# Kernel optimization log

Hardware: AMD Instinct MI355X
Metric: run time of the kernel (lower is better)

## Reference

```python
import jax, jax.numpy as jnp
import numpy as np

MARGIN = 0.3
BIG = 1e6  # matches the 1000000.0 additive mask in the torch code


def setup_inputs() -> dict:
    key = jax.random.key(0)
    k1, k2 = jax.random.split(key)
    embeddings = jax.random.normal(k1, (4096, 512), dtype=jnp.float32)
    labels = jax.random.randint(k2, (4096,), 0, 512)
    return {"embeddings": embeddings, "labels": labels}


def reference(embeddings, labels):
    # Pairwise euclidean distances (torch.cdist p=2) via the GEMM identity,
    # clamped before sqrt for numerical safety on the zero diagonal.
    sq = jnp.sum(embeddings * embeddings, axis=1)                      # [N]
    d2 = sq[:, None] + sq[None, :] - 2.0 * (embeddings @ embeddings.T)  # [N, N]
    dist = jnp.sqrt(jnp.maximum(d2, 1e-12))

    pos_mask = labels[None, :] == labels[:, None]   # [N, N] bool
    neg_mask = ~pos_mask

    # Hardest positive per anchor (self-distance 0 is harmless under max).
    hp = jnp.max(dist * pos_mask.astype(dist.dtype), axis=1)           # [N]

    # Semi-hard negatives: hp < d(a, n) < hp + margin, different label.
    semi_hard = (dist > hp[:, None]) & (dist < hp[:, None] + MARGIN) & neg_mask
    has_semi_hard = jnp.sum(semi_hard) > 0

    # Fallback: hardest (farthest) negative; semi-hard branch: closest semi-hard.
    hn_fallback = jnp.max(dist * neg_mask.astype(dist.dtype), axis=1)
    hn_semi = jnp.min(dist + (1.0 - semi_hard.astype(dist.dtype)) * BIG, axis=1)
    hn = jnp.where(has_semi_hard, hn_semi, hn_fallback)                # [N]

    triplet = jax.nn.relu(hp - hn + MARGIN)                            # [N]
    num_valid = jnp.sum((triplet > 0).astype(triplet.dtype))
    loss = jnp.where(num_valid > 0,
                     jnp.sum(triplet) / jnp.maximum(num_valid, 1.0),
                     jnp.mean(triplet))
    return loss
```

## Files before the change

kernel.cpp:

```cpp
#include <hip/hip_runtime.h>
#include <math.h>


constexpr float MARGIN = 0.3f;

typedef _Float16 half8    __attribute__((ext_vector_type(8)));
typedef float    floatx16 __attribute__((ext_vector_type(16)));

#define GLD_LDS16(gp, lp)                                                              \
    __builtin_amdgcn_global_load_lds(                                                  \
        (const __attribute__((address_space(1))) void*)(gp),                           \
        (__attribute__((address_space(3))) void*)(lp), 16, 0, 0)

__global__ __launch_bounds__(256)
void prep_kernel(const float* __restrict__ e, _Float16* __restrict__ pan,
                 float* __restrict__ sq, unsigned int* __restrict__ hp,
                 unsigned int* __restrict__ hn_fall, unsigned int* __restrict__ hn_semi,
                 unsigned int* __restrict__ bars, int N, int D) {
    __shared__ float red[256];
    if (blockIdx.x == 0 && threadIdx.x < 32) bars[threadIdx.x * 32] = 0u;
    const int r0  = blockIdx.x * 8;
    const int p   = r0 >> 7;
    const int rl  = r0 & 127;
    const int r   = threadIdx.x & 7;
    const int c8  = threadIdx.x >> 3;
    const int row = r0 + r;
    const float* er = e + (size_t)row * D;
    float s = 0.f;
    #pragma unroll
    for (int it = 0; it < 2; ++it) {
        const int kw = c8 + it * 32;
        const float4 x0 = *(const float4*)&er[kw * 8];
        const float4 x1 = *(const float4*)&er[kw * 8 + 4];
        const float xv[8] = {x0.x, x0.y, x0.z, x0.w, x1.x, x1.y, x1.z, x1.w};
        half8 hi, lo;
        #pragma unroll
        for (int jj = 0; jj < 8; ++jj) {
            _Float16 h = (_Float16)xv[jj];
            hi[jj] = h;
            lo[jj] = (_Float16)(xv[jj] - (float)h);
            s += xv[jj] * xv[jj];
        }
        *(half8*)&pan[((size_t)(p * 128 + kw) * 128 + rl + r) * 8]      = hi;
        *(half8*)&pan[((size_t)(p * 128 + 64 + kw) * 128 + rl + r) * 8] = lo;
    }
    red[threadIdx.x] = s;
    __syncthreads();
    if (threadIdx.x < 8) {
        float t = 0.f;
        #pragma unroll
        for (int c = 0; c < 32; ++c) t += red[threadIdx.x + 8 * c];
        const int rw = r0 + threadIdx.x;
        sq[rw]      = t;
        hp[rw]      = 0u;
        hn_fall[rw] = 0u;
        hn_semi[rw] = 0x7f800000u;
    }
}

__global__ __launch_bounds__(512, 2)
void fused_kernel(const _Float16* __restrict__ pan, const int* __restrict__ labels,
                  const float* __restrict__ sq,
                  unsigned int* __restrict__ hp,
                  unsigned int* __restrict__ hn_fall,
                  unsigned int* __restrict__ hn_semi,
                  unsigned int* __restrict__ bars,
                  float* __restrict__ out,
                  int N, int D, unsigned int nrowblocks, unsigned int nblocks) {
    __shared__ __attribute__((aligned(16))) _Float16 S[2][32768];
    __shared__ float sq_r[256], sq_c[256], hp_r[256];
    __shared__ int   lab_r[256], lab_c[256];
    __shared__ int   lastflag;

    const int tid  = threadIdx.x;
    const int lane = tid & 63;
    const int wave = tid >> 6;
    const int wr   = (wave >> 2) * 128;
    const int wcol = (wave & 3) * 64;
    const int mrow = lane & 31;
    const int half_id = lane >> 5;

    const int j  = blockIdx.x & 7;
    const int i  = blockIdx.x >> 3;
    const int px = (j & 3) * 4 + (i & 3);
    const int py = (j >> 2) * 8 + (i >> 2);
    const int rowBase = py * 256;
    const int colBase = px * 256;

    if (tid < 256) {
        sq_r[tid]  = sq[rowBase + tid];
        lab_r[tid] = labels[rowBase + tid];
    } else {
        const int t2 = tid - 256;
        sq_c[t2]  = sq[colBase + t2];
        lab_c[t2] = labels[colBase + t2];
    }

    floatx16 acc[2][4];
    #pragma unroll
    for (int b = 0; b < 2; ++b)
        #pragma unroll
        for (int a = 0; a < 4; ++a)
            #pragma unroll
            for (int r = 0; r < 16; ++r) acc[b][a][r] = 0.f;

    auto stage_slab = [&](int nxt, int t, int u) {
        const int s = wave * 8 + u;
        int kcl, pp, rowin, lofs;
        if (s < 32) {
            kcl = s >> 2; const int rq = s & 3;
            pp    = 2 * py + (rq >> 1);
            rowin = (rq & 1) * 64 + lane;
            lofs  = (kcl * 256 + rq * 64) * 8;
        } else {
            const int u2 = s - 32;
            kcl = u2 >> 2; const int cq = u2 & 3;
            pp    = 2 * px + (cq >> 1);
            rowin = (cq & 1) * 64 + lane;
            lofs  = 16384 + (kcl * 256 + cq * 64) * 8;
        }
        const int kc = (kcl < 4) ? (4 * t + kcl) : (64 + 4 * t + (kcl - 4));
        const _Float16* g = pan + ((size_t)(pp * 128 + kc) * 128 + rowin) * 8;
        GLD_LDS16(g, &S[nxt][lofs]);
    };

    #pragma unroll
    for (int u = 0; u < 8; ++u) stage_slab(0, 0, u);
    __syncthreads();

    #pragma unroll 1
    for (int t = 0; t < 16; ++t) {
        const int cur = t & 1, nxt = cur ^ 1;
        const _Float16* Sc = &S[cur][0];
        half8 ah[4], bh[2];
        #pragma unroll
        for (int ph = 0; ph < 4; ++ph) {
            const int kbase = (ph >> 1) * 2 + (ph & 1) * 4;
            half8 av[4], bv[2];
            #pragma unroll
            for (int ai = 0; ai < 4; ++ai)
                av[ai] = *(const half8*)&Sc[((kbase + half_id) * 256 + wr + ai * 32 + mrow) * 8];
            #pragma unroll
            for (int bj = 0; bj < 2; ++bj)
                bv[bj] = *(const half8*)&Sc[16384 + ((kbase + half_id) * 256 + wcol + bj * 32 + mrow) * 8];
            if (t + 1 < 16) {
                stage_slab(nxt, t + 1, 2 * ph);
                stage_slab(nxt, t + 1, 2 * ph + 1);
            }
            asm volatile("" ::: "memory");
            __builtin_amdgcn_s_barrier();
            asm volatile("" ::: "memory");
            __builtin_amdgcn_s_setprio(1);
            if ((ph & 1) == 0) {
                #pragma unroll
                for (int bj = 0; bj < 2; ++bj)
                    #pragma unroll
                    for (int ai = 0; ai < 4; ++ai)
                        acc[bj][ai] = __builtin_amdgcn_mfma_f32_32x32x16_f16(
                            bv[bj], av[ai], acc[bj][ai], 0, 0, 0);
                #pragma unroll
                for (int ai = 0; ai < 4; ++ai) ah[ai] = av[ai];
                bh[0] = bv[0]; bh[1] = bv[1];
            } else {
                #pragma unroll
                for (int bj = 0; bj < 2; ++bj)
                    #pragma unroll
                    for (int ai = 0; ai < 4; ++ai)
                        acc[bj][ai] = __builtin_amdgcn_mfma_f32_32x32x16_f16(
                            bh[bj], av[ai], acc[bj][ai], 0, 0, 0);
                #pragma unroll
                for (int bj = 0; bj < 2; ++bj)
                    #pragma unroll
                    for (int ai = 0; ai < 4; ++ai)
                        acc[bj][ai] = __builtin_amdgcn_mfma_f32_32x32x16_f16(
                            bv[bj], ah[ai], acc[bj][ai], 0, 0, 0);
            }
            __builtin_amdgcn_s_setprio(0);
            if (ph == 3) { asm volatile("s_waitcnt vmcnt(0)" ::: "memory"); }
            asm volatile("" ::: "memory");
            __builtin_amdgcn_s_barrier();
            asm volatile("" ::: "memory");
        }
    }

    float sqr[4]; int labr[4];
    #pragma unroll
    for (int ai = 0; ai < 4; ++ai) {
        sqr[ai]  = sq_r[wr + ai * 32 + mrow];
        labr[ai] = lab_r[wr + ai * 32 + mrow];
    }

    #pragma unroll
    for (int ai = 0; ai < 4; ++ai) {
        float vp = 0.f, vn = 0.f;
        #pragma unroll
        for (int bj = 0; bj < 2; ++bj) {
            #pragma unroll
            for (int r = 0; r < 16; ++r) {
                const int c = wcol + bj * 32 + (r & 3) + 8 * (r >> 2) + 4 * half_id;
                float d = sqrtf(fmaxf(sqr[ai] + sq_c[c] - 2.0f * acc[bj][ai][r], 1e-12f));
                const bool pos = (labr[ai] == lab_c[c]);
                vp = fmaxf(vp, pos ? d : 0.f);
                vn = fmaxf(vn, pos ? 0.f : d);
            }
        }
        vp = fmaxf(vp, __shfl_xor(vp, 32, 64));
        vn = fmaxf(vn, __shfl_xor(vn, 32, 64));
        if (half_id == 0) {
            atomicMax(&hp[rowBase + wr + ai * 32 + mrow],      __float_as_uint(vp));
            atomicMax(&hn_fall[rowBase + wr + ai * 32 + mrow], __float_as_uint(vn));
        }
    }

    __syncthreads();
    unsigned int* ctr = &bars[py * 32];
    if (tid == 0) {
        __threadfence();
        atomicAdd(ctr, 1u);
        while (__hip_atomic_load(ctr, __ATOMIC_ACQUIRE, __HIP_MEMORY_SCOPE_AGENT)
               < nrowblocks)
            __builtin_amdgcn_s_sleep(32);
    }
    __syncthreads();
    if (tid < 256)
        hp_r[tid] = __uint_as_float(__hip_atomic_load(&hp[rowBase + tid],
                                    __ATOMIC_RELAXED, __HIP_MEMORY_SCOPE_AGENT));
    __syncthreads();

    #pragma unroll
    for (int ai = 0; ai < 4; ++ai) {
        const float hpv = hp_r[wr + ai * 32 + mrow];
        float vm = __builtin_inff();
        #pragma unroll
        for (int bj = 0; bj < 2; ++bj) {
            #pragma unroll
            for (int r = 0; r < 16; ++r) {
                const int c = wcol + bj * 32 + (r & 3) + 8 * (r >> 2) + 4 * half_id;
                float d = sqrtf(fmaxf(sqr[ai] + sq_c[c] - 2.0f * acc[bj][ai][r], 1e-12f));
                const bool cand = (labr[ai] != lab_c[c]) && (d > hpv);
                vm = fminf(vm, cand ? d : __builtin_inff());
            }
        }
        vm = fminf(vm, __shfl_xor(vm, 32, 64));
        if (half_id == 0)
            atomicMin(&hn_semi[rowBase + wr + ai * 32 + mrow], __float_as_uint(vm));
    }

    __syncthreads();
    if (tid == 0) {
        __threadfence();
        unsigned int old = atomicAdd(&bars[992], 1u);
        lastflag = (old == nblocks - 1) ? 1 : 0;
    }
    __syncthreads();
    if (!lastflag) return;
    if (tid == 0) __threadfence();
    __syncthreads();

    float* FS = (float*)&S[0][0];
    int*   IC = (int*)(FS + 512);
    int*   IA = IC + 512;
    int any = 0;
    for (int r = tid; r < N; r += 512) {
        float h  = __uint_as_float(__hip_atomic_load(&hp[r],      __ATOMIC_RELAXED, __HIP_MEMORY_SCOPE_AGENT));
        float hs = __uint_as_float(__hip_atomic_load(&hn_semi[r], __ATOMIC_RELAXED, __HIP_MEMORY_SCOPE_AGENT));
        any |= (hs < h + MARGIN) ? 1 : 0;
    }
    IA[tid] = any;
    __syncthreads();
    for (int s = 256; s; s >>= 1) {
        if (tid < s) IA[tid] |= IA[tid + s];
        __syncthreads();
    }
    const bool has_semi = IA[0] != 0;
    float sum = 0.f; int valid = 0;
    for (int r = tid; r < N; r += 512) {
        float h  = __uint_as_float(__hip_atomic_load(&hp[r], __ATOMIC_RELAXED, __HIP_MEMORY_SCOPE_AGENT));
        float hn = has_semi
            ? __uint_as_float(__hip_atomic_load(&hn_semi[r], __ATOMIC_RELAXED, __HIP_MEMORY_SCOPE_AGENT))
            : __uint_as_float(__hip_atomic_load(&hn_fall[r], __ATOMIC_RELAXED, __HIP_MEMORY_SCOPE_AGENT));
        float t = fmaxf(h - hn + MARGIN, 0.f);
        if (!(t > 0.f)) t = 0.f;
        sum += t;
        valid += (t > 0.f) ? 1 : 0;
    }
    FS[tid] = sum; IC[tid] = valid;
    __syncthreads();
    for (int s = 256; s; s >>= 1) {
        if (tid < s) { FS[tid] += FS[tid + s]; IC[tid] += IC[tid + s]; }
        __syncthreads();
    }
    if (tid == 0) {
        float total = FS[0]; int v = IC[0];
        out[0] = (v > 0) ? (total / (float)v) : (total / (float)N);
    }
}

extern "C" void kernel_launch(void* const* d_in, const int* in_sizes, int n_in,
                              void* d_out, int out_size, void* d_ws, size_t ws_size,
                              hipStream_t stream) {
    const float* e      = (const float*)d_in[0];
    const int*   labels = (const int*)d_in[1];
    const int N = in_sizes[1];
    const int D = in_sizes[0] / N;
    float* out = (float*)d_out;

    float*        sq      = (float*)d_ws;
    unsigned int* hp      = (unsigned int*)d_ws + N;
    unsigned int* hn_fall = hp + N;
    unsigned int* hn_semi = hn_fall + N;
    unsigned int* bars    = hn_semi + N;

    const size_t small_bytes = ((size_t)(4 * N + 1024) * 4 + 255) & ~(size_t)255;
    _Float16* pan = (_Float16*)((char*)d_ws + small_bytes);

    prep_kernel<<<N / 8, 256, 0, stream>>>(e, pan, sq, hp, hn_fall, hn_semi, bars, N, D);

    const int ntx = N / 256, nty = N / 256;
    fused_kernel<<<ntx * nty, 512, 0, stream>>>(pan, labels, sq, hp, hn_fall, hn_semi,
                                                bars, out, N, D,
                                                (unsigned)ntx, (unsigned)(ntx * nty));
}
```

Measured before the change: 140.1 us.

## Use 4-wave blocks with 128x128 per-wave tiles and whole-slab prefetch

Halves the block size to 256 threads so each wave computes a 128x128 output sub-tile (4x4 MFMA accumulators) instead of 128x64. The next K-slab is now issued all at once at the top of each iteration, and the fine-grained per-phase barriers are replaced by a single wait and barrier per iteration. The goal is more MFMA reuse per LDS read and less synchronisation. The cost is twice the accumulator registers per wave and lower occupancy (launch bounds 256,1), which may reduce latency hiding.

```diff
diff --git a/kernel.cpp b/kernel.cpp
--- a/kernel.cpp
+++ b/kernel.cpp
@@ -58,7 +58,7 @@
     }
 }
 
-__global__ __launch_bounds__(512, 2)
+__global__ __launch_bounds__(256, 1)
 void fused_kernel(const _Float16* __restrict__ pan, const int* __restrict__ labels,
                   const float* __restrict__ sq,
                   unsigned int* __restrict__ hp,
@@ -75,8 +75,8 @@
     const int tid  = threadIdx.x;
     const int lane = tid & 63;
     const int wave = tid >> 6;
-    const int wr   = (wave >> 2) * 128;
-    const int wcol = (wave & 3) * 64;
+    const int wr   = (wave >> 1) * 128;
+    const int wcol = (wave & 1) * 128;
     const int mrow = lane & 31;
     const int half_id = lane >> 5;
 
@@ -87,25 +87,21 @@
     const int rowBase = py * 256;
     const int colBase = px * 256;
 
-    if (tid < 256) {
-        sq_r[tid]  = sq[rowBase + tid];
-        lab_r[tid] = labels[rowBase + tid];
-    } else {
-        const int t2 = tid - 256;
-        sq_c[t2]  = sq[colBase + t2];
-        lab_c[t2] = labels[colBase + t2];
-    }
-
-    floatx16 acc[2][4];
-    #pragma unroll
-    for (int b = 0; b < 2; ++b)
+    sq_r[tid]  = sq[rowBase + tid];
+    lab_r[tid] = labels[rowBase + tid];
+    sq_c[tid]  = sq[colBase + tid];
+    lab_c[tid] = labels[colBase + tid];
+
+    floatx16 acc[4][4];
+    #pragma unroll
+    for (int b = 0; b < 4; ++b)
         #pragma unroll
         for (int a = 0; a < 4; ++a)
             #pragma unroll
             for (int r = 0; r < 16; ++r) acc[b][a][r] = 0.f;
 
-    auto stage_slab = [&](int nxt, int t, int u) {
-        const int s = wave * 8 + u;
+    auto stage_slab = [&](int buf, int t, int u) {
+        const int s = wave * 16 + u;
         int kcl, pp, rowin, lofs;
         if (s < 32) {
             kcl = s >> 2; const int rq = s & 3;
@@ -121,66 +117,59 @@
         }
         const int kc = (kcl < 4) ? (4 * t + kcl) : (64 + 4 * t + (kcl - 4));
         const _Float16* g = pan + ((size_t)(pp * 128 + kc) * 128 + rowin) * 8;
-        GLD_LDS16(g, &S[nxt][lofs]);
+        GLD_LDS16(g, &S[buf][lofs]);
     };
 
     #pragma unroll
-    for (int u = 0; u < 8; ++u) stage_slab(0, 0, u);
+    for (int u = 0; u < 16; ++u) stage_slab(0, 0, u);
     __syncthreads();
 
     #pragma unroll 1
     for (int t = 0; t < 16; ++t) {
-        const int cur = t & 1, nxt = cur ^ 1;
+        const int cur = t & 1;
         const _Float16* Sc = &S[cur][0];
-        half8 ah[4], bh[2];
-        #pragma unroll
-        for (int ph = 0; ph < 4; ++ph) {
-            const int kbase = (ph >> 1) * 2 + (ph & 1) * 4;
-            half8 av[4], bv[2];
+        if (t + 1 < 16) {
+            #pragma unroll
+            for (int u = 0; u < 16; ++u) stage_slab(cur ^ 1, t + 1, u);
+        }
+        auto rdA = [&](half8* a, int kbase) {
             #pragma unroll
             for (int ai = 0; ai < 4; ++ai)
-                av[ai] = *(const half8*)&Sc[((kbase + half_id) * 256 + wr + ai * 32 + mrow) * 8];
-            #pragma unroll
-            for (int bj = 0; bj < 2; ++bj)
-                bv[bj] = *(const half8*)&Sc[16384 + ((kbase + half_id) * 256 + wcol + bj * 32 + mrow) * 8];
-            if (t + 1 < 16) {
-                stage_slab(nxt, t + 1, 2 * ph);
-                stage_slab(nxt, t + 1, 2 * ph + 1);
-            }
-            asm volatile("" ::: "memory");
-            __builtin_amdgcn_s_barrier();
-            asm volatile("" ::: "memory");
-            __builtin_amdgcn_s_setprio(1);
-            if ((ph & 1) == 0) {
+                a[ai] = *(const half8*)&Sc[((kbase + half_id) * 256 + wr + ai * 32 + mrow) * 8];
+        };
+        auto rdB = [&](half8* bq, int kbase) {
+            #pragma unroll
+            for (int bj = 0; bj < 4; ++bj)
+                bq[bj] = *(const half8*)&Sc[16384 + ((kbase + half_id) * 256 + wcol + bj * 32 + mrow) * 8];
+        };
+        auto mm = [&](const half8* bq, const half8* aq) {
+            #pragma unroll
+            for (int bj = 0; bj < 4; ++bj)
                 #pragma unroll
-                for (int bj = 0; bj < 2; ++bj)
-                    #pragma unroll
-                    for (int ai = 0; ai < 4; ++ai)
-                        acc[bj][ai] = __builtin_amdgcn_mfma_f32_32x32x16_f16(
-                            bv[bj], av[ai], acc[bj][ai], 0, 0, 0);
-                #pragma unroll
-                for (int ai = 0; ai < 4; ++ai) ah[ai] = av[ai];
-                bh[0] = bv[0]; bh[1] = bv[1];
-            } else {
-                #pragma unroll
-                for (int bj = 0; bj < 2; ++bj)
-                    #pragma unroll
-                    for (int ai = 0; ai < 4; ++ai)
-                        acc[bj][ai] = __builtin_amdgcn_mfma_f32_32x32x16_f16(
-                            bh[bj], av[ai], acc[bj][ai], 0, 0, 0);
-                #pragma unroll
-                for (int bj = 0; bj < 2; ++bj)
-                    #pragma unroll
-                    for (int ai = 0; ai < 4; ++ai)
-                        acc[bj][ai] = __builtin_amdgcn_mfma_f32_32x32x16_f16(
-                            bv[bj], ah[ai], acc[bj][ai], 0, 0, 0);
-            }
-            __builtin_amdgcn_s_setprio(0);
-            if (ph == 3) { asm volatile("s_waitcnt vmcnt(0)" ::: "memory"); }
-            asm volatile("" ::: "memory");
-            __builtin_amdgcn_s_barrier();
-            asm volatile("" ::: "memory");
-        }
+                for (int ai = 0; ai < 4; ++ai)
+                    acc[bj][ai] = __builtin_amdgcn_mfma_f32_32x32x16_f16(
+                        bq[bj], aq[ai], acc[bj][ai], 0, 0, 0);
+        };
+        half8 ah0[4], bh0[4], al0[4], bl0[4], ah1[4], bh1[4], al1[4], bl1[4];
+        rdA(ah0, 0); rdB(bh0, 0);
+        rdA(al0, 4); rdB(bl0, 4);
+        __builtin_amdgcn_s_setprio(1);
+        mm(bh0, ah0);
+        __builtin_amdgcn_s_setprio(0);
+        rdA(ah1, 2); rdB(bh1, 2);
+        __builtin_amdgcn_s_setprio(1);
+        mm(bh0, al0);
+        mm(bl0, ah0);
+        __builtin_amdgcn_s_setprio(0);
+        rdA(al1, 6); rdB(bl1, 6);
+        __builtin_amdgcn_s_setprio(1);
+        mm(bh1, ah1);
+        mm(bh1, al1);
+        mm(bl1, ah1);
+        __builtin_amdgcn_s_setprio(0);
+        asm volatile("s_waitcnt vmcnt(0)" ::: "memory");
+        __builtin_amdgcn_s_barrier();
+        asm volatile("" ::: "memory");
     }
 
     float sqr[4]; int labr[4];
@@ -194,7 +183,7 @@
     for (int ai = 0; ai < 4; ++ai) {
         float vp = 0.f, vn = 0.f;
         #pragma unroll
-        for (int bj = 0; bj < 2; ++bj) {
+        for (int bj = 0; bj < 4; ++bj) {
             #pragma unroll
             for (int r = 0; r < 16; ++r) {
                 const int c = wcol + bj * 32 + (r & 3) + 8 * (r >> 2) + 4 * half_id;
@@ -222,9 +211,8 @@
             __builtin_amdgcn_s_sleep(32);
     }
     __syncthreads();
-    if (tid < 256)
-        hp_r[tid] = __uint_as_float(__hip_atomic_load(&hp[rowBase + tid],
-                                    __ATOMIC_RELAXED, __HIP_MEMORY_SCOPE_AGENT));
+    hp_r[tid] = __uint_as_float(__hip_atomic_load(&hp[rowBase + tid],
+                                __ATOMIC_RELAXED, __HIP_MEMORY_SCOPE_AGENT));
     __syncthreads();
 
     #pragma unroll
@@ -232,7 +220,7 @@
         const float hpv = hp_r[wr + ai * 32 + mrow];
         float vm = __builtin_inff();
         #pragma unroll
-        for (int bj = 0; bj < 2; ++bj) {
+        for (int bj = 0; bj < 4; ++bj) {
             #pragma unroll
             for (int r = 0; r < 16; ++r) {
                 const int c = wcol + bj * 32 + (r & 3) + 8 * (r >> 2) + 4 * half_id;
@@ -258,23 +246,23 @@
     __syncthreads();
 
     float* FS = (float*)&S[0][0];
-    int*   IC = (int*)(FS + 512);
-    int*   IA = IC + 512;
+    int*   IC = (int*)(FS + 256);
+    int*   IA = IC + 256;
     int any = 0;
-    for (int r = tid; r < N; r += 512) {
+    for (int r = tid; r < N; r += 256) {
         float h  = __uint_as_float(__hip_atomic_load(&hp[r],      __ATOMIC_RELAXED, __HIP_MEMORY_SCOPE_AGENT));
         float hs = __uint_as_float(__hip_atomic_load(&hn_semi[r], __ATOMIC_RELAXED, __HIP_MEMORY_SCOPE_AGENT));
         any |= (hs < h + MARGIN) ? 1 : 0;
     }
     IA[tid] = any;
     __syncthreads();
-    for (int s = 256; s; s >>= 1) {
+    for (int s = 128; s; s >>= 1) {
         if (tid < s) IA[tid] |= IA[tid + s];
         __syncthreads();
     }
     const bool has_semi = IA[0] != 0;
     float sum = 0.f; int valid = 0;
-    for (int r = tid; r < N; r += 512) {
+    for (int r = tid; r < N; r += 256) {
         float h  = __uint_as_float(__hip_atomic_load(&hp[r], __ATOMIC_RELAXED, __HIP_MEMORY_SCOPE_AGENT));
         float hn = has_semi
             ? __uint_as_float(__hip_atomic_load(&hn_semi[r], __ATOMIC_RELAXED, __HIP_MEMORY_SCOPE_AGENT))
@@ -286,7 +274,7 @@
     }
     FS[tid] = sum; IC[tid] = valid;
     __syncthreads();
-    for (int s = 256; s; s >>= 1) {
+    for (int s = 128; s; s >>= 1) {
         if (tid < s) { FS[tid] += FS[tid + s]; IC[tid] += IC[tid + s]; }
         __syncthreads();
     }
@@ -317,7 +305,7 @@
     prep_kernel<<<N / 8, 256, 0, stream>>>(e, pan, sq, hp, hn_fall, hn_semi, bars, N, D);
 
     const int ntx = N / 256, nty = N / 256;
-    fused_kernel<<<ntx * nty, 512, 0, stream>>>(pan, labels, sq, hp, hn_fall, hn_semi,
+    fused_kernel<<<ntx * nty, 256, 0, stream>>>(pan, labels, sq, hp, hn_fall, hn_semi,
                                                 bars, out, N, D,
                                                 (unsigned)ntx, (unsigned)(ntx * nty));
 }
```

Result: slower. 228.8 us (+63.4%).

## Issue whole next-slab prefetch upfront and cut per-phase barriers in GEMM loop

Applied to the files above, without the earlier changes.

Restructures the main K loop of the fused distance GEMM. All eight global-to-LDS slab loads for the next stage are issued at the start of each iteration, and the two half-k chunks are processed with full hi/lo fragment loads. This removes the two barriers per phase in favour of one wait-and-barrier per iteration, reducing synchronisation stalls. The trade-off is that loads are no longer interleaved with MFMA phases, and more fragment registers are live at once.

```diff
diff --git a/kernel.cpp b/kernel.cpp
--- a/kernel.cpp
+++ b/kernel.cpp
@@ -104,7 +104,7 @@
             #pragma unroll
             for (int r = 0; r < 16; ++r) acc[b][a][r] = 0.f;
 
-    auto stage_slab = [&](int nxt, int t, int u) {
+    auto stage_slab = [&](int buf, int t, int u) {
         const int s = wave * 8 + u;
         int kcl, pp, rowin, lofs;
         if (s < 32) {
@@ -121,7 +121,7 @@
         }
         const int kc = (kcl < 4) ? (4 * t + kcl) : (64 + 4 * t + (kcl - 4));
         const _Float16* g = pan + ((size_t)(pp * 128 + kc) * 128 + rowin) * 8;
-        GLD_LDS16(g, &S[nxt][lofs]);
+        GLD_LDS16(g, &S[buf][lofs]);
     };
 
     #pragma unroll
@@ -130,57 +130,45 @@
 
     #pragma unroll 1
     for (int t = 0; t < 16; ++t) {
-        const int cur = t & 1, nxt = cur ^ 1;
+        const int cur = t & 1;
         const _Float16* Sc = &S[cur][0];
-        half8 ah[4], bh[2];
-        #pragma unroll
-        for (int ph = 0; ph < 4; ++ph) {
-            const int kbase = (ph >> 1) * 2 + (ph & 1) * 4;
-            half8 av[4], bv[2];
+        if (t + 1 < 16) {
+            #pragma unroll
+            for (int u = 0; u < 8; ++u) stage_slab(cur ^ 1, t + 1, u);
+        }
+        auto mm = [&](const half8* bq, const half8* aq) {
+            #pragma unroll
+            for (int bj = 0; bj < 2; ++bj)
+                #pragma unroll
+                for (int ai = 0; ai < 4; ++ai)
+                    acc[bj][ai] = __builtin_amdgcn_mfma_f32_32x32x16_f16(
+                        bq[bj], aq[ai], acc[bj][ai], 0, 0, 0);
+        };
+        #pragma unroll
+        for (int ks = 0; ks < 2; ++ks) {
+            const int kb = 2 * ks;
+            half8 ah[4], bh[2], al[4], bl[2];
             #pragma unroll
             for (int ai = 0; ai < 4; ++ai)
-                av[ai] = *(const half8*)&Sc[((kbase + half_id) * 256 + wr + ai * 32 + mrow) * 8];
+                ah[ai] = *(const half8*)&Sc[((kb + half_id) * 256 + wr + ai * 32 + mrow) * 8];
             #pragma unroll
             for (int bj = 0; bj < 2; ++bj)
-                bv[bj] = *(const half8*)&Sc[16384 + ((kbase + half_id) * 256 + wcol + bj * 32 + mrow) * 8];
-            if (t + 1 < 16) {
-                stage_slab(nxt, t + 1, 2 * ph);
-                stage_slab(nxt, t + 1, 2 * ph + 1);
-            }
-            asm volatile("" ::: "memory");
-            __builtin_amdgcn_s_barrier();
-            asm volatile("" ::: "memory");
+                bh[bj] = *(const half8*)&Sc[16384 + ((kb + half_id) * 256 + wcol + bj * 32 + mrow) * 8];
+            #pragma unroll
+            for (int ai = 0; ai < 4; ++ai)
+                al[ai] = *(const half8*)&Sc[((4 + kb + half_id) * 256 + wr + ai * 32 + mrow) * 8];
+            #pragma unroll
+            for (int bj = 0; bj < 2; ++bj)
+                bl[bj] = *(const half8*)&Sc[16384 + ((4 + kb + half_id) * 256 + wcol + bj * 32 + mrow) * 8];
             __builtin_amdgcn_s_setprio(1);
-            if ((ph & 1) == 0) {
-                #pragma unroll
-                for (int bj = 0; bj < 2; ++bj)
-                    #pragma unroll
-                    for (int ai = 0; ai < 4; ++ai)
-                        acc[bj][ai] = __builtin_amdgcn_mfma_f32_32x32x16_f16(
-                            bv[bj], av[ai], acc[bj][ai], 0, 0, 0);
-                #pragma unroll
-                for (int ai = 0; ai < 4; ++ai) ah[ai] = av[ai];
-                bh[0] = bv[0]; bh[1] = bv[1];
-            } else {
-                #pragma unroll
-                for (int bj = 0; bj < 2; ++bj)
-                    #pragma unroll
-                    for (int ai = 0; ai < 4; ++ai)
-                        acc[bj][ai] = __builtin_amdgcn_mfma_f32_32x32x16_f16(
-                            bh[bj], av[ai], acc[bj][ai], 0, 0, 0);
-                #pragma unroll
-                for (int bj = 0; bj < 2; ++bj)
-                    #pragma unroll
-                    for (int ai = 0; ai < 4; ++ai)
-                        acc[bj][ai] = __builtin_amdgcn_mfma_f32_32x32x16_f16(
-                            bv[bj], ah[ai], acc[bj][ai], 0, 0, 0);
-            }
+            mm(bh, ah);
+            mm(bh, al);
+            mm(bl, ah);
             __builtin_amdgcn_s_setprio(0);
-            if (ph == 3) { asm volatile("s_waitcnt vmcnt(0)" ::: "memory"); }
-            asm volatile("" ::: "memory");
-            __builtin_amdgcn_s_barrier();
-            asm volatile("" ::: "memory");
-        }
+        }
+        asm volatile("s_waitcnt vmcnt(0)" ::: "memory");
+        __builtin_amdgcn_s_barrier();
+        asm volatile("" ::: "memory");
     }
 
     float sqr[4]; int labr[4];
```

New measurement: 137.5 us. No clear change (-1.9%).
